# Kernel optimization log

Hardware: AMD Instinct MI355X
Metric: run time of the kernel (lower is better)

## Reference

```python
import jax, jax.numpy as jnp
import numpy as np

N = 30000   # fluid particles
E = 480000  # edges
F = 4       # fluidFeatures (in channels)
P = 8       # RBF basis size per dim (dims=[8], 1D)
LAYERS = [32, 64, 64, 2]


def hat_basis(x, n):
    # 'linear' RBF: hat functions on n evenly spaced centers in [-1, 1]
    centers = jnp.linspace(-1.0, 1.0, n, dtype=x.dtype)
    spacing = 2.0 / (n - 1)
    return jnp.maximum(0.0, 1.0 - jnp.abs(x[:, None] - centers[None, :]) / spacing)  # [E, n]


def rbf_conv(x, fi, fj, d, W, b, mask, n_nodes):
    # x: [N, Cin]; d: [E, 1] clamped; W: [P, Cin, Cout]; b: [Cout]
    phi = hat_basis(d[:, 0], W.shape[0])      # [E, P]
    xj = x[fj]                                 # gather source features [E, Cin]
    msg = jnp.zeros((xj.shape[0], W.shape[2]), dtype=x.dtype)
    for p in range(W.shape[0]):                # small fixed P=8 loop keeps memory O(E*Cout)
        msg = msg + phi[:, p, None] * (xj @ W[p])
    msg = jnp.where(mask[:, None], msg, 0.0)   # centerIgnore: drop self edges fi==fj
    out = jax.ops.segment_sum(msg, fi, num_segments=n_nodes)  # scatter-reduce to targets
    return out + b


def _xavier(key, shape_in, shape_out):
    lim = float(np.sqrt(6.0 / (shape_in + shape_out)))
    return jax.random.uniform(key, (shape_in, shape_out), jnp.float32, -lim, lim)


def setup_inputs() -> dict:
    key = jax.random.key(0)
    ks = jax.random.split(key, 16)
    fluidFeatures = jax.random.normal(ks[0], (N, F), jnp.float32)
    fi = jax.random.randint(ks[1], (E,), 0, N)
    fj = jax.random.randint(ks[2], (E,), 0, N)
    distances = jax.random.normal(ks[3], (E, 1), jnp.float32)
    # conv channels: 4->32, 64->64, 64->64, 64->2
    cio = [(F, 32), (2 * 32, 64), (64, 64), (64, 2)]
    inp = {"fluidFeatures": fluidFeatures, "fi": fi, "fj": fj, "distances": distances}
    for li, (ci, co) in enumerate(cio):
        inp[f"cW{li}"] = jax.random.normal(ks[4 + li], (P, ci, co), jnp.float32) * (1.0 / np.sqrt(P * ci))
        inp[f"cb{li}"] = jnp.zeros((co,), jnp.float32)
        inp[f"fW{li}"] = _xavier(ks[8 + li], ci, co)   # stored [in, out]
        inp[f"fb{li}"] = jnp.zeros((co,), jnp.float32)
    return inp


def reference(fluidFeatures, fi, fj, distances,
              cW0, cb0, fW0, fb0, cW1, cb1, fW1, fb1,
              cW2, cb2, fW2, fb2, cW3, cb3, fW3, fb3):
    n_nodes = fluidFeatures.shape[0]
    mask = fi != fj                     # centerIgnore (mask instead of filter: jit-safe)
    d = jnp.clip(distances, -1.0, 1.0)

    conv0 = rbf_conv(fluidFeatures, fi, fj, d, cW0, cb0, mask, n_nodes)  # [N, 32]
    lin0 = fluidFeatures @ fW0 + fb0                                      # [N, 32]
    ans = jnp.concatenate([lin0, conv0], axis=1)                          # [N, 64]

    # i = 1: features[0]=32 != features[1]=64 -> no residual
    ansc = jax.nn.relu(ans)
    ans = rbf_conv(ansc, fi, fj, d, cW1, cb1, mask, n_nodes) + (ansc @ fW1 + fb1)
    # i = 2: features[1]==features[2]==64 and shapes match -> residual
    ansc = jax.nn.relu(ans)
    ans = rbf_conv(ansc, fi, fj, d, cW2, cb2, mask, n_nodes) + (ansc @ fW2 + fb2) + ans
    # i = 3: 64 -> 2, no residual
    ansc = jax.nn.relu(ans)
    ans = rbf_conv(ansc, fi, fj, d, cW3, cb3, mask, n_nodes) + (ansc @ fW3 + fb3)

    return ans  # dim == 1 (dims=[8]) -> no /128
```

## Files before the change

kernel.cpp:

```cpp
#include <hip/hip_runtime.h>


#define CAP 48

typedef __attribute__((ext_vector_type(8))) short short8;
typedef __attribute__((ext_vector_type(4))) float f32x4;
typedef int v4i __attribute__((ext_vector_type(4)));

__device__ __forceinline__ short bf16s(float f) {
  unsigned u = __float_as_uint(f);
  return (short)((u + 0x7FFF + ((u >> 16) & 1)) >> 16);
}
__device__ __forceinline__ float b2f(unsigned short s) {
  return __uint_as_float(((unsigned)s) << 16);
}
__device__ __forceinline__ unsigned pack2(float a, float b) {
  return (unsigned)(unsigned short)bf16s(a) | ((unsigned)(unsigned short)bf16s(b) << 16);
}
__device__ __forceinline__ float dec_w0(int v) {
  return __uint_as_float(0x3F800000u | (((unsigned)v & 0xFFFu) << 11)) - 1.0f;
}
__device__ __forceinline__ float dec_sf(int v) {
  return (float)(((unsigned)v >> 12) & 1u);
}
__device__ __forceinline__ unsigned long long rfl64(unsigned long long x) {
  unsigned lo = __builtin_amdgcn_readfirstlane((unsigned)x);
  unsigned hi = __builtin_amdgcn_readfirstlane((unsigned)(x >> 32));
  return ((unsigned long long)hi << 32) | (unsigned long long)lo;
}

#define LOAD_RECS32Q(JROW, CPTR, MRAW)                                      \
  v4i q0, q1, q2, q3, q4, q5, q6, q7;                                       \
  int MRAW;                                                                 \
  asm volatile("s_load_dwordx4 %0, %9, 0x0\n\t"                             \
               "s_load_dwordx4 %1, %9, 0x10\n\t"                            \
               "s_load_dwordx4 %2, %9, 0x20\n\t"                            \
               "s_load_dwordx4 %3, %9, 0x30\n\t"                            \
               "s_load_dwordx4 %4, %9, 0x40\n\t"                            \
               "s_load_dwordx4 %5, %9, 0x50\n\t"                            \
               "s_load_dwordx4 %6, %9, 0x60\n\t"                            \
               "s_load_dwordx4 %7, %9, 0x70\n\t"                            \
               "s_load_dword %8, %10, 0x0\n\t"                              \
               "s_waitcnt lgkmcnt(0)"                                       \
               : "=&s"(q0), "=&s"(q1), "=&s"(q2), "=&s"(q3), "=&s"(q4),     \
                 "=&s"(q5), "=&s"(q6), "=&s"(q7), "=&s"(MRAW)               \
               : "s"(JROW), "s"(CPTR)                                       \
               : "memory")

#define LOAD_RECS16TQ(JROW)                                                 \
  v4i qt0, qt1, qt2, qt3;                                                   \
  asm volatile("s_load_dwordx4 %0, %4, 0x80\n\t"                            \
               "s_load_dwordx4 %1, %4, 0x90\n\t"                            \
               "s_load_dwordx4 %2, %4, 0xA0\n\t"                            \
               "s_load_dwordx4 %3, %4, 0xB0\n\t"                            \
               "s_waitcnt lgkmcnt(0)"                                       \
               : "=&s"(qt0), "=&s"(qt1), "=&s"(qt2), "=&s"(qt3)             \
               : "s"(JROW)                                                  \
               : "memory")

#define RECK(K) ((K) < 4 ? q0[(K) & 3] : (K) < 8 ? q1[(K) & 3] :            \
                 (K) < 12 ? q2[(K) & 3] : (K) < 16 ? q3[(K) & 3] :          \
                 (K) < 20 ? q4[(K) & 3] : (K) < 24 ? q5[(K) & 3] :          \
                 (K) < 28 ? q6[(K) & 3] : q7[(K) & 3])
#define RECT(K) ((K) < 4 ? qt0[(K) & 3] : (K) < 8 ? qt1[(K) & 3] :          \
                 (K) < 12 ? qt2[(K) & 3] : qt3[(K) & 3])

__global__ void fill_prep(const float* __restrict__ dist,
                          const int* __restrict__ fi, const int* __restrict__ fj,
                          int* __restrict__ cnt, int* __restrict__ jw, int nE,
                          const float* __restrict__ cW0, const float* __restrict__ fW0,
                          const float* __restrict__ cb0, const float* __restrict__ fb0,
                          const float* __restrict__ cW1, const float* __restrict__ fW1,
                          const float* __restrict__ cb1, const float* __restrict__ fb1,
                          const float* __restrict__ cW2, const float* __restrict__ fW2,
                          const float* __restrict__ cb2, const float* __restrict__ fb2,
                          const float* __restrict__ cW3,
                          short* __restrict__ W0T, short* __restrict__ W1T,
                          short* __restrict__ W2T, short* __restrict__ WT3,
                          float* __restrict__ BIA,
                          const float* __restrict__ X,
                          unsigned short* __restrict__ Xb, int n,
                          int fillBlocks, int prepBlocks) {
  if ((int)blockIdx.x < fillBlocks) {
    int e = blockIdx.x * blockDim.x + threadIdx.x;
    if (e >= nE) return;
    int i = fi[e], j = fj[e];
    if (i == j) return;
    float d = fminf(1.0f, fmaxf(-1.0f, dist[e]));
    float u = (d + 1.0f) * 3.5f;
    int p = min((int)u, 6);
    float w0 = 1.0f - (u - (float)p);
    int wq = min((int)(w0 * 4096.0f + 0.5f), 4095);
    int pos = atomicAdd(&cnt[i], 1);
    if (pos < CAP)
      jw[(size_t)i * CAP + pos] =
          (int)(((unsigned)j << 17) | ((unsigned)p << 14) | 0x1000u | (unsigned)wq);
  } else if ((int)blockIdx.x < fillBlocks + prepBlocks) {
    int idx = ((int)blockIdx.x - fillBlocks) * blockDim.x + threadIdx.x;
    if (idx < 36864) {
      int o = idx / 576, k = idx - o * 576;
      float v = (k < 512) ? cW1[((size_t)(k >> 6) * 64 + (k & 63)) * 64 + o]
                          : fW1[(size_t)(k - 512) * 64 + o];
      W1T[idx] = bf16s(v);
    } else if (idx < 73728) {
      int r = idx - 36864;
      int o = r / 576, k = r - o * 576;
      float v = (k < 512) ? cW2[((size_t)(k >> 6) * 64 + (k & 63)) * 64 + o]
                          : fW2[(size_t)(k - 512) * 64 + o];
      W2T[r] = bf16s(v);
    } else if (idx < 110592) {
      int r = idx - 73728;
      int o = r / 576, k = r - o * 576;
      float v = 0.0f;
      if (k < 512) {
        int s = k >> 6, ci = k & 63;
        if (ci < 4 && o >= 32) v = cW0[((size_t)s * 4 + ci) * 32 + (o - 32)];
      } else {
        int c = k - 512;
        if (c < 4 && o < 32) v = fW0[(size_t)c * 32 + o];
      }
      W0T[r] = bf16s(v);
    } else if (idx < 111616) {
      int r = idx - 110592;
      int t = r >> 6, ch = r & 63;
      WT3[r] = bf16s(cW3[((size_t)(t >> 1) * 64 + ch) * 2 + (t & 1)]);
    } else if (idx < 111808) {
      int r = idx - 111616;
      int layer = r >> 6, ch = r & 63;
      float v;
      if (layer == 0) v = (ch < 32) ? fb0[ch] : cb0[ch - 32];
      else if (layer == 1) v = cb1[ch] + fb1[ch];
      else v = cb2[ch] + fb2[ch];
      BIA[r] = v;
    }
  } else {
    int idx = ((int)blockIdx.x - fillBlocks - prepBlocks) * blockDim.x + threadIdx.x;
    if (idx >= n * 8) return;
    int i = idx >> 3, g = idx & 7;
    uint4 val = make_uint4(0u, 0u, 0u, 0u);
    if (g == 0) {
      float4 x = *(const float4*)(X + (size_t)i * 4);
      val.x = pack2(x.x, x.y);
      val.y = pack2(x.z, x.w);
    }
    *(uint4*)(Xb + (size_t)i * 64 + g * 8) = val;
  }
}

__global__ __launch_bounds__(1024, 8) void conv_agg(
    const unsigned short* __restrict__ prev,
    const int* __restrict__ cnt, const int* __restrict__ jw,
    const short* __restrict__ WTn,
    const float* __restrict__ bias,
    const float* __restrict__ resid,
    float* __restrict__ outF32,
    unsigned short* __restrict__ outAnsc,
    const short* __restrict__ WT3,
    float* __restrict__ T, int flags, int n) {
  __shared__ __align__(16) unsigned short sA[16 * 584];
  __shared__ __align__(16) unsigned short sC[16 * 72];
  const int tid = threadIdx.x;
  const int w = tid >> 6;
  const int lane = tid & 63;
  const unsigned ln2 = (unsigned)lane * 2u;
  const int nodeBase = blockIdx.x * 16;
  const int i = nodeBase + w;
  const bool valid = (i < n);
  const int ic = valid ? i : 0;
  const int* jrow = (const int*)rfl64((unsigned long long)(jw + (size_t)ic * CAP));
  const int* cptr = (const int*)rfl64((unsigned long long)(cnt + ic));
  LOAD_RECS32Q(jrow, cptr, mraw);
  const int m = valid ? min(mraw, CAP) : 0;
  const unsigned short own = prev[(size_t)ic * 64 + lane];
  float aS0 = 0, aS1 = 0, aS2 = 0, aS3 = 0, aS4 = 0, aS5 = 0, aS6 = 0, aS7 = 0;
  unsigned u0, u1, u2, u3, u4, u5, u6, u7;
  unsigned u8, u9, u10, u11, u12, u13, u14, u15;
#define GSETU(G, V) { int v_ = (V);                                         \
    u##G = ((((unsigned)v_) >> 10) & 0xFFFFFF80u) + ln2; }
#define GISSUE16_W8(BASE)                                                   \
  asm volatile("global_load_ushort %0, %0, %[bb]\n\t"                       \
               "global_load_ushort %1, %1, %[bb]\n\t"                       \
               "global_load_ushort %2, %2, %[bb]\n\t"                       \
               "global_load_ushort %3, %3, %[bb]\n\t"                       \
               "global_load_ushort %4, %4, %[bb]\n\t"                       \
               "global_load_ushort %5, %5, %[bb]\n\t"                       \
               "global_load_ushort %6, %6, %[bb]\n\t"                       \
               "global_load_ushort %7, %7, %[bb]\n\t"                       \
               "global_load_ushort %8, %8, %[bb]\n\t"                       \
               "global_load_ushort %9, %9, %[bb]\n\t"                       \
               "global_load_ushort %10, %10, %[bb]\n\t"                     \
               "global_load_ushort %11, %11, %[bb]\n\t"                     \
               "global_load_ushort %12, %12, %[bb]\n\t"                     \
               "global_load_ushort %13, %13, %[bb]\n\t"                     \
               "global_load_ushort %14, %14, %[bb]\n\t"                     \
               "global_load_ushort %15, %15, %[bb]\n\t"                     \
               "s_waitcnt vmcnt(8)"                                         \
               : "+v"(u0), "+v"(u1), "+v"(u2), "+v"(u3),                    \
                 "+v"(u4), "+v"(u5), "+v"(u6), "+v"(u7),                    \
                 "+v"(u8), "+v"(u9), "+v"(u10), "+v"(u11),                  \
                 "+v"(u12), "+v"(u13), "+v"(u14), "+v"(u15)                 \
               : [bb] "s"(BASE)                                             \
               : "memory")
#define WAITV0_HI                                                           \
  asm volatile("s_waitcnt vmcnt(0)"                                         \
               : "+v"(u8), "+v"(u9), "+v"(u10), "+v"(u11),                  \
                 "+v"(u12), "+v"(u13), "+v"(u14), "+v"(u15)                 \
               :: "memory")
#define GCONSU(G, V) { int v_ = (V);                                        \
    float w0_ = dec_w0(v_);                                                 \
    float w1_ = dec_sf(v_) - w0_;                                           \
    float xv_ = __uint_as_float(u##G << 16);                                \
    switch ((((unsigned)v_) >> 14) & 7u) {                                  \
      case 0: aS0 = fmaf(w0_, xv_, aS0); aS1 = fmaf(w1_, xv_, aS1); break;  \
      case 1: aS1 = fmaf(w0_, xv_, aS1); aS2 = fmaf(w1_, xv_, aS2); break;  \
      case 2: aS2 = fmaf(w0_, xv_, aS2); aS3 = fmaf(w1_, xv_, aS3); break;  \
      case 3: aS3 = fmaf(w0_, xv_, aS3); aS4 = fmaf(w1_, xv_, aS4); break;  \
      case 4: aS4 = fmaf(w0_, xv_, aS4); aS5 = fmaf(w1_, xv_, aS5); break;  \
      case 5: aS5 = fmaf(w0_, xv_, aS5); aS6 = fmaf(w1_, xv_, aS6); break;  \
      case 6: aS6 = fmaf(w0_, xv_, aS6); aS7 = fmaf(w1_, xv_, aS7); break;  \
      default: break;                                                       \
    } }
  GSETU(0, RECK(0))   GSETU(1, RECK(1))   GSETU(2, RECK(2))   GSETU(3, RECK(3))
  GSETU(4, RECK(4))   GSETU(5, RECK(5))   GSETU(6, RECK(6))   GSETU(7, RECK(7))
  GSETU(8, RECK(8))   GSETU(9, RECK(9))   GSETU(10, RECK(10)) GSETU(11, RECK(11))
  GSETU(12, RECK(12)) GSETU(13, RECK(13)) GSETU(14, RECK(14)) GSETU(15, RECK(15))
  GISSUE16_W8(prev);
  GCONSU(0, RECK(0)) GCONSU(1, RECK(1)) GCONSU(2, RECK(2)) GCONSU(3, RECK(3))
  GCONSU(4, RECK(4)) GCONSU(5, RECK(5)) GCONSU(6, RECK(6)) GCONSU(7, RECK(7))
  WAITV0_HI;
  GCONSU(8, RECK(8))   GCONSU(9, RECK(9))   GCONSU(10, RECK(10))
  GCONSU(11, RECK(11)) GCONSU(12, RECK(12)) GCONSU(13, RECK(13))
  GCONSU(14, RECK(14)) GCONSU(15, RECK(15))
  if (m > 16) {
    GSETU(0, RECK(16))  GSETU(1, RECK(17))  GSETU(2, RECK(18))  GSETU(3, RECK(19))
    GSETU(4, RECK(20))  GSETU(5, RECK(21))  GSETU(6, RECK(22))  GSETU(7, RECK(23))
    GSETU(8, RECK(24))  GSETU(9, RECK(25))  GSETU(10, RECK(26)) GSETU(11, RECK(27))
    GSETU(12, RECK(28)) GSETU(13, RECK(29)) GSETU(14, RECK(30)) GSETU(15, RECK(31))
    GISSUE16_W8(prev);
    GCONSU(0, RECK(16)) GCONSU(1, RECK(17)) GCONSU(2, RECK(18)) GCONSU(3, RECK(19))
    GCONSU(4, RECK(20)) GCONSU(5, RECK(21)) GCONSU(6, RECK(22)) GCONSU(7, RECK(23))
    WAITV0_HI;
    GCONSU(8, RECK(24))  GCONSU(9, RECK(25))  GCONSU(10, RECK(26))
    GCONSU(11, RECK(27)) GCONSU(12, RECK(28)) GCONSU(13, RECK(29))
    GCONSU(14, RECK(30)) GCONSU(15, RECK(31))
    if (m > 32) {
      LOAD_RECS16TQ(jrow);
      GSETU(0, RECT(0))   GSETU(1, RECT(1))   GSETU(2, RECT(2))   GSETU(3, RECT(3))
      GSETU(4, RECT(4))   GSETU(5, RECT(5))   GSETU(6, RECT(6))   GSETU(7, RECT(7))
      GSETU(8, RECT(8))   GSETU(9, RECT(9))   GSETU(10, RECT(10)) GSETU(11, RECT(11))
      GSETU(12, RECT(12)) GSETU(13, RECT(13)) GSETU(14, RECT(14)) GSETU(15, RECT(15))
      GISSUE16_W8(prev);
      GCONSU(0, RECT(0)) GCONSU(1, RECT(1)) GCONSU(2, RECT(2)) GCONSU(3, RECT(3))
      GCONSU(4, RECT(4)) GCONSU(5, RECT(5)) GCONSU(6, RECT(6)) GCONSU(7, RECT(7))
      WAITV0_HI;
      GCONSU(8, RECT(8))   GCONSU(9, RECT(9))   GCONSU(10, RECT(10))
      GCONSU(11, RECT(11)) GCONSU(12, RECT(12)) GCONSU(13, RECT(13))
      GCONSU(14, RECT(14)) GCONSU(15, RECT(15))
    }
  }
#undef GSETU
#undef GISSUE16_W8
#undef WAITV0_HI
#undef GCONSU
  {
    unsigned short* sAr = sA + w * 584;
    sAr[0 * 64 + lane] = (unsigned short)bf16s(aS0);
    sAr[1 * 64 + lane] = (unsigned short)bf16s(aS1);
    sAr[2 * 64 + lane] = (unsigned short)bf16s(aS2);
    sAr[3 * 64 + lane] = (unsigned short)bf16s(aS3);
    sAr[4 * 64 + lane] = (unsigned short)bf16s(aS4);
    sAr[5 * 64 + lane] = (unsigned short)bf16s(aS5);
    sAr[6 * 64 + lane] = (unsigned short)bf16s(aS6);
    sAr[7 * 64 + lane] = (unsigned short)bf16s(aS7);
    sAr[512 + lane] = own;
  }
  __syncthreads();

  if (w < 4) {
    const int mrow = lane & 15, quad = lane >> 4, t = w;
    const unsigned rowoff = (unsigned)((t * 16 + mrow) * 1152 + quad * 16);
    const unsigned short* brow = sA + mrow * 584 + quad * 8;
    f32x4 acc4 = {0, 0, 0, 0};
    short8 f0, f1, f2, f3, f4, f5;
#define WLOAD6(CO)                                                          \
  asm volatile("global_load_dwordx4 %0, %[vo], %[bb] offset:0\n\t"          \
               "global_load_dwordx4 %1, %[vo], %[bb] offset:64\n\t"         \
               "global_load_dwordx4 %2, %[vo], %[bb] offset:128\n\t"        \
               "global_load_dwordx4 %3, %[vo], %[bb] offset:192\n\t"        \
               "global_load_dwordx4 %4, %[vo], %[bb] offset:256\n\t"        \
               "global_load_dwordx4 %5, %[vo], %[bb] offset:320\n\t"        \
               "s_waitcnt vmcnt(0)"                                         \
               : "=&v"(f0), "=&v"(f1), "=&v"(f2), "=&v"(f3),                \
                 "=&v"(f4), "=&v"(f5)                                       \
               : [vo] "v"(rowoff + (CO)), [bb] "s"(WTn)                     \
               : "memory")
#define MM6(KK0)                                                            \
  acc4 = __builtin_amdgcn_mfma_f32_16x16x32_bf16(                           \
      f0, *(const short8*)(brow + ((KK0) + 0) * 32), acc4, 0, 0, 0);        \
  acc4 = __builtin_amdgcn_mfma_f32_16x16x32_bf16(                           \
      f1, *(const short8*)(brow + ((KK0) + 1) * 32), acc4, 0, 0, 0);        \
  acc4 = __builtin_amdgcn_mfma_f32_16x16x32_bf16(                           \
      f2, *(const short8*)(brow + ((KK0) + 2) * 32), acc4, 0, 0, 0);        \
  acc4 = __builtin_amdgcn_mfma_f32_16x16x32_bf16(                           \
      f3, *(const short8*)(brow + ((KK0) + 3) * 32), acc4, 0, 0, 0);        \
  acc4 = __builtin_amdgcn_mfma_f32_16x16x32_bf16(                           \
      f4, *(const short8*)(brow + ((KK0) + 4) * 32), acc4, 0, 0, 0);        \
  acc4 = __builtin_amdgcn_mfma_f32_16x16x32_bf16(                           \
      f5, *(const short8*)(brow + ((KK0) + 5) * 32), acc4, 0, 0, 0);
    WLOAD6(0);    MM6(0);
    WLOAD6(384);  MM6(6);
    WLOAD6(768);  MM6(12);
#undef WLOAD6
#undef MM6
    const int node2 = nodeBase + mrow;
    const int ch0 = t * 16 + quad * 4;
    if (node2 < n) {
      float4 bb4 = *(const float4*)(bias + ch0);
      float4 rv = make_float4(0.f, 0.f, 0.f, 0.f);
      if (flags & 1) rv = *(const float4*)(resid + (size_t)node2 * 64 + ch0);
      float o0 = acc4[0] + bb4.x + rv.x;
      float o1 = acc4[1] + bb4.y + rv.y;
      float o2 = acc4[2] + bb4.z + rv.z;
      float o3 = acc4[3] + bb4.w + rv.w;
      if (flags & 2) {
        *(float2*)(outF32 + (size_t)node2 * 64 + ch0) = make_float2(o0, o1);
        *(float2*)(outF32 + (size_t)node2 * 64 + ch0 + 2) = make_float2(o2, o3);
      }
      unsigned lo = pack2(fmaxf(o0, 0.f), fmaxf(o1, 0.f));
      unsigned hi = pack2(fmaxf(o2, 0.f), fmaxf(o3, 0.f));
      *(uint2*)(outAnsc + (size_t)node2 * 64 + ch0) = make_uint2(lo, hi);
      if (flags & 4) {
        *(unsigned*)(sC + mrow * 72 + ch0) = lo;
        *(unsigned*)(sC + mrow * 72 + ch0 + 2) = hi;
      }
    } else if (flags & 4) {
      *(unsigned*)(sC + mrow * 72 + ch0) = 0u;
      *(unsigned*)(sC + mrow * 72 + ch0 + 2) = 0u;
    }
  }
  if (flags & 4) {
    __syncthreads();
    if (w == 0) {
      const int mrow = lane & 15, quad = lane >> 4;
      short8 b0 = *(const short8*)(sC + mrow * 72 + quad * 8);
      short8 b1 = *(const short8*)(sC + mrow * 72 + quad * 8 + 32);
      short8 a0v = *(const short8*)(WT3 + mrow * 64 + quad * 8);
      short8 a1v = *(const short8*)(WT3 + mrow * 64 + quad * 8 + 32);
      f32x4 acc4 = {0, 0, 0, 0};
      acc4 = __builtin_amdgcn_mfma_f32_16x16x32_bf16(a0v, b0, acc4, 0, 0, 0);
      acc4 = __builtin_amdgcn_mfma_f32_16x16x32_bf16(a1v, b1, acc4, 0, 0, 0);
      const int node2 = nodeBase + mrow;
      if (node2 < n) {
        float* tr = T + (size_t)node2 * 18 + quad * 4;
        *(float2*)(tr) = make_float2(acc4[0], acc4[1]);
        *(float2*)(tr + 2) = make_float2(acc4[2], acc4[3]);
      }
    }
  }
}

__global__ __launch_bounds__(256, 4) void layer3_kernel(
    const unsigned short* __restrict__ Xb,
    const float* __restrict__ T,
    const int* __restrict__ cnt, const int* __restrict__ jw,
    const float* __restrict__ cb3, const float* __restrict__ fb3,
    const float* __restrict__ fW3,
    float* __restrict__ out, int n) {
  const int lane = threadIdx.x & 63;
  const int i = (blockIdx.x * blockDim.x + threadIdx.x) >> 6;
  if (i >= n) return;
  const int m = min(cnt[i], CAP);
  float c0 = 0.0f, c1 = 0.0f;
  if (lane < m) {
    int v = jw[(size_t)i * CAP + lane];
    unsigned j = (unsigned)v >> 17;
    unsigned p = ((unsigned)v >> 14) & 7u;
    unsigned off9 = j * 9u + p;
    float w0 = dec_w0(v);
    float w1 = 1.0f - w0;
    const float* tb = T + (size_t)off9 * 2;
    float2 ta = *(const float2*)(tb);
    float2 tc = *(const float2*)(tb + 2);
    c0 = w0 * ta.x + w1 * tc.x;
    c1 = w0 * ta.y + w1 * tc.y;
  }
  float xi = b2f(Xb[(size_t)i * 64 + lane]);
  float2 fw = *(const float2*)(fW3 + lane * 2);
  c0 = fmaf(xi, fw.x, c0);
  c1 = fmaf(xi, fw.y, c1);
  #pragma unroll
  for (int off = 32; off > 0; off >>= 1) {
    c0 += __shfl_xor(c0, off, 64);
    c1 += __shfl_xor(c1, off, 64);
  }
  if (lane == 0) {
    out[(size_t)i * 2 + 0] = c0 + cb3[0] + fb3[0];
    out[(size_t)i * 2 + 1] = c1 + cb3[1] + fb3[1];
  }
}

extern "C" void kernel_launch(void* const* d_in, const int* in_sizes, int n_in,
                              void* d_out, int out_size, void* d_ws, size_t ws_size,
                              hipStream_t stream) {
  const float* X    = (const float*)d_in[0];
  const int*   fi   = (const int*)d_in[1];
  const int*   fj   = (const int*)d_in[2];
  const float* dist = (const float*)d_in[3];
  const float* cW0 = (const float*)d_in[4];  const float* cb0 = (const float*)d_in[5];
  const float* fW0 = (const float*)d_in[6];  const float* fb0 = (const float*)d_in[7];
  const float* cW1 = (const float*)d_in[8];  const float* cb1 = (const float*)d_in[9];
  const float* fW1 = (const float*)d_in[10]; const float* fb1 = (const float*)d_in[11];
  const float* cW2 = (const float*)d_in[12]; const float* cb2 = (const float*)d_in[13];
  const float* fW2 = (const float*)d_in[14]; const float* fb2 = (const float*)d_in[15];
  const float* cW3 = (const float*)d_in[16]; const float* cb3 = (const float*)d_in[17];
  const float* fW3 = (const float*)d_in[18]; const float* fb3 = (const float*)d_in[19];
  float* out = (float*)d_out;

  const int n  = in_sizes[0] / 4;
  const int nE = in_sizes[1];

  unsigned short* ansc0 = (unsigned short*)d_ws;
  float*          ans1  = (float*)(ansc0 + (size_t)n * 64);
  unsigned short* ansc1 = (unsigned short*)(ans1 + (size_t)n * 64);
  unsigned short* ansc2 = ansc1 + (size_t)n * 64;
  float*          T     = (float*)(ansc2 + (size_t)n * 64);
  unsigned short* Xb16  = (unsigned short*)(T + (size_t)n * 18);
  short* W1T = (short*)(Xb16 + (size_t)n * 64);
  short* W2T = W1T + 36864;
  short* W0T = W2T + 36864;
  short* WT3 = W0T + 36864;
  float* BIA = (float*)(WT3 + 1024);
  int*   jw  = (int*)(BIA + 192);
  int*   cnt = jw + (size_t)n * CAP;

  hipMemsetAsync(jw, 0, ((size_t)n * CAP + n) * sizeof(int), stream);
  const int fillBlocks = (nE + 255) / 256;
  const int prepBlocks = (111808 + 255) / 256;
  const int xbBlocks   = (n * 8 + 255) / 256;
  fill_prep<<<fillBlocks + prepBlocks + xbBlocks, 256, 0, stream>>>(
      dist, fi, fj, cnt, jw, nE,
      cW0, fW0, cb0, fb0, cW1, fW1, cb1, fb1, cW2, fW2, cb2, fb2, cW3,
      W0T, W1T, W2T, WT3, BIA, X, Xb16, n, fillBlocks, prepBlocks);

  const int nodeBlocks = (n + 15) / 16;
  conv_agg<<<nodeBlocks, 1024, 0, stream>>>(Xb16, cnt, jw, W0T, BIA,
                                            ans1, ans1, ansc0, WT3, T, 0, n);
  conv_agg<<<nodeBlocks, 1024, 0, stream>>>(ansc0, cnt, jw, W1T, BIA + 64,
                                            ans1, ans1, ansc1, WT3, T, 2, n);
  conv_agg<<<nodeBlocks, 1024, 0, stream>>>(ansc1, cnt, jw, W2T, BIA + 128,
                                            ans1, ans1, ansc2, WT3, T, 5, n);
  layer3_kernel<<<(n * 64 + 255) / 256, 256, 0, stream>>>(ansc2, T, cnt, jw,
                                                          cb3, fb3, fW3, out, n);
}
```

Before: 249.4 us.

## Bucket edges by RBF bin and accumulate sorted runs in conv_agg

Edge records are first bucketed per node by basis index p into a 128-slot staging array, then a new compact kernel writes them into the per-node CAP list sorted by p. conv_agg then walks edges in p order with two running accumulators and flushes them to shared memory on each bin change, replacing the 8-way switch over eight accumulator registers. Edges past the count are masked, and the weight quantisation grows to 14 bits. This adds a kernel launch and extra staging memory traffic, and the flush branches may diverge across edges.

Result: no change. 245.5 us (-1.6%).

```diff
diff --git a/kernel.cpp b/kernel.cpp
--- a/kernel.cpp
+++ b/kernel.cpp
@@ -17,11 +17,8 @@
 __device__ __forceinline__ unsigned pack2(float a, float b) {
   return (unsigned)(unsigned short)bf16s(a) | ((unsigned)(unsigned short)bf16s(b) << 16);
 }
-__device__ __forceinline__ float dec_w0(int v) {
-  return __uint_as_float(0x3F800000u | (((unsigned)v & 0xFFFu) << 11)) - 1.0f;
-}
-__device__ __forceinline__ float dec_sf(int v) {
-  return (float)(((unsigned)v >> 12) & 1u);
+__device__ __forceinline__ float dec14(int v) {
+  return __uint_as_float(0x3F800000u | (((unsigned)v & 0x3FFFu) << 9)) - 1.0f;
 }
 __device__ __forceinline__ unsigned long long rfl64(unsigned long long x) {
   unsigned lo = __builtin_amdgcn_readfirstlane((unsigned)x);
@@ -67,7 +64,7 @@
 
 __global__ void fill_prep(const float* __restrict__ dist,
                           const int* __restrict__ fi, const int* __restrict__ fj,
-                          int* __restrict__ cnt, int* __restrict__ jw, int nE,
+                          int* __restrict__ cnt8, int* __restrict__ jwB, int nE,
                           const float* __restrict__ cW0, const float* __restrict__ fW0,
                           const float* __restrict__ cb0, const float* __restrict__ fb0,
                           const float* __restrict__ cW1, const float* __restrict__ fW1,
@@ -90,11 +87,11 @@
     float u = (d + 1.0f) * 3.5f;
     int p = min((int)u, 6);
     float w0 = 1.0f - (u - (float)p);
-    int wq = min((int)(w0 * 4096.0f + 0.5f), 4095);
-    int pos = atomicAdd(&cnt[i], 1);
-    if (pos < CAP)
-      jw[(size_t)i * CAP + pos] =
-          (int)(((unsigned)j << 17) | ((unsigned)p << 14) | 0x1000u | (unsigned)wq);
+    int wq = min((int)(w0 * 16384.0f + 0.5f), 16383);
+    int pos = atomicAdd(&cnt8[i * 8 + p], 1);
+    if (pos < 16)
+      jwB[(size_t)i * 128 + p * 16 + pos] =
+          (int)(((unsigned)j << 17) | ((unsigned)p << 14) | (unsigned)wq);
   } else if ((int)blockIdx.x < fillBlocks + prepBlocks) {
     int idx = ((int)blockIdx.x - fillBlocks) * blockDim.x + threadIdx.x;
     if (idx < 36864) {
@@ -147,6 +144,34 @@
   }
 }
 
+__global__ __launch_bounds__(256, 8) void compact_kernel(
+    const int* __restrict__ jwB, const int* __restrict__ cnt8,
+    int* __restrict__ jw, int* __restrict__ cnt, int n) {
+  const int w = threadIdx.x >> 6, lane = threadIdx.x & 63;
+  const int i = blockIdx.x * 4 + w;
+  if (i >= n) return;
+  const int4* c8 = (const int4*)(cnt8 + (size_t)i * 8);
+  int4 ca = c8[0], cb = c8[1];
+  int c0 = min(ca.x, 16), c1 = min(ca.y, 16), c2 = min(ca.z, 16), c3 = min(ca.w, 16);
+  int c4 = min(cb.x, 16), c5 = min(cb.y, 16), c6 = min(cb.z, 16), c7 = min(cb.w, 16);
+  int tot = c0 + c1 + c2 + c3 + c4 + c5 + c6 + c7;
+  if (lane == 0) cnt[i] = min(tot, CAP);
+  #pragma unroll
+  for (int h = 0; h < 2; ++h) {
+    int s = lane + h * 64;
+    int p = s >> 4, k = s & 15;
+    int cp = p == 0 ? c0 : p == 1 ? c1 : p == 2 ? c2 : p == 3 ? c3
+           : p == 4 ? c4 : p == 5 ? c5 : p == 6 ? c6 : c7;
+    int ps = (p > 0 ? c0 : 0) + (p > 1 ? c1 : 0) + (p > 2 ? c2 : 0) +
+             (p > 3 ? c3 : 0) + (p > 4 ? c4 : 0) + (p > 5 ? c5 : 0) +
+             (p > 6 ? c6 : 0);
+    if (k < cp) {
+      int pos = ps + k;
+      if (pos < CAP) jw[(size_t)i * CAP + pos] = jwB[(size_t)i * 128 + s];
+    }
+  }
+}
+
 __global__ __launch_bounds__(1024, 8) void conv_agg(
     const unsigned short* __restrict__ prev,
     const int* __restrict__ cnt, const int* __restrict__ jw,
@@ -170,13 +195,18 @@
   const int* jrow = (const int*)rfl64((unsigned long long)(jw + (size_t)ic * CAP));
   const int* cptr = (const int*)rfl64((unsigned long long)(cnt + ic));
   LOAD_RECS32Q(jrow, cptr, mraw);
-  const int m = valid ? min(mraw, CAP) : 0;
+  const int mloc = valid ? min(mraw, CAP) : 0;
   const unsigned short own = prev[(size_t)ic * 64 + lane];
-  float aS0 = 0, aS1 = 0, aS2 = 0, aS3 = 0, aS4 = 0, aS5 = 0, aS6 = 0, aS7 = 0;
+  unsigned short* sAr = sA + w * 584;
+  #pragma unroll
+  for (int r = 0; r < 8; ++r) sAr[r * 64 + lane] = 0;
+  sAr[512 + lane] = own;
   unsigned u0, u1, u2, u3, u4, u5, u6, u7;
   unsigned u8, u9, u10, u11, u12, u13, u14, u15;
-#define GSETU(G, V) { int v_ = (V);                                         \
-    u##G = ((((unsigned)v_) >> 10) & 0xFFFFFF80u) + ln2; }
+#define GSETU(G, KCMP, RV)                                                  \
+  { unsigned o_ = ((KCMP) < mloc)                                           \
+        ? ((((unsigned)(RV)) >> 10) & 0xFFFFFF80u) : 0u;                    \
+    u##G = o_ + ln2; }
 #define GISSUE16_W8(BASE)                                                   \
   asm volatile("global_load_ushort %0, %0, %[bb]\n\t"                       \
                "global_load_ushort %1, %1, %[bb]\n\t"                       \
@@ -206,74 +236,80 @@
                : "+v"(u8), "+v"(u9), "+v"(u10), "+v"(u11),                  \
                  "+v"(u12), "+v"(u13), "+v"(u14), "+v"(u15)                 \
                :: "memory")
-#define GCONSU(G, V) { int v_ = (V);                                        \
-    float w0_ = dec_w0(v_);                                                 \
-    float w1_ = dec_sf(v_) - w0_;                                           \
+#define CONSK(KCMP, G, RV)                                                  \
+  if ((KCMP) == mloc) goto cons_done;                                       \
+  { int v_ = (RV);                                                          \
+    int pk_ = (v_ >> 14) & 7;                                               \
+    if (pk_ != pcur) {                                                      \
+      sAr[pcur * 64 + lane] = (unsigned short)bf16s(curA);                  \
+      if (pk_ == pcur + 1) { curA = curB; }                                 \
+      else { sAr[(pcur + 1) * 64 + lane] = (unsigned short)bf16s(curB);     \
+             curA = 0.0f; }                                                 \
+      curB = 0.0f; pcur = pk_;                                              \
+    }                                                                       \
+    float f_ = __uint_as_float(0x3F800000u | (((unsigned)v_ & 0x3FFFu) << 9)); \
     float xv_ = __uint_as_float(u##G << 16);                                \
-    switch ((((unsigned)v_) >> 14) & 7u) {                                  \
-      case 0: aS0 = fmaf(w0_, xv_, aS0); aS1 = fmaf(w1_, xv_, aS1); break;  \
-      case 1: aS1 = fmaf(w0_, xv_, aS1); aS2 = fmaf(w1_, xv_, aS2); break;  \
-      case 2: aS2 = fmaf(w0_, xv_, aS2); aS3 = fmaf(w1_, xv_, aS3); break;  \
-      case 3: aS3 = fmaf(w0_, xv_, aS3); aS4 = fmaf(w1_, xv_, aS4); break;  \
-      case 4: aS4 = fmaf(w0_, xv_, aS4); aS5 = fmaf(w1_, xv_, aS5); break;  \
-      case 5: aS5 = fmaf(w0_, xv_, aS5); aS6 = fmaf(w1_, xv_, aS6); break;  \
-      case 6: aS6 = fmaf(w0_, xv_, aS6); aS7 = fmaf(w1_, xv_, aS7); break;  \
-      default: break;                                                       \
-    } }
-  GSETU(0, RECK(0))   GSETU(1, RECK(1))   GSETU(2, RECK(2))   GSETU(3, RECK(3))
-  GSETU(4, RECK(4))   GSETU(5, RECK(5))   GSETU(6, RECK(6))   GSETU(7, RECK(7))
-  GSETU(8, RECK(8))   GSETU(9, RECK(9))   GSETU(10, RECK(10)) GSETU(11, RECK(11))
-  GSETU(12, RECK(12)) GSETU(13, RECK(13)) GSETU(14, RECK(14)) GSETU(15, RECK(15))
-  GISSUE16_W8(prev);
-  GCONSU(0, RECK(0)) GCONSU(1, RECK(1)) GCONSU(2, RECK(2)) GCONSU(3, RECK(3))
-  GCONSU(4, RECK(4)) GCONSU(5, RECK(5)) GCONSU(6, RECK(6)) GCONSU(7, RECK(7))
-  WAITV0_HI;
-  GCONSU(8, RECK(8))   GCONSU(9, RECK(9))   GCONSU(10, RECK(10))
-  GCONSU(11, RECK(11)) GCONSU(12, RECK(12)) GCONSU(13, RECK(13))
-  GCONSU(14, RECK(14)) GCONSU(15, RECK(15))
-  if (m > 16) {
-    GSETU(0, RECK(16))  GSETU(1, RECK(17))  GSETU(2, RECK(18))  GSETU(3, RECK(19))
-    GSETU(4, RECK(20))  GSETU(5, RECK(21))  GSETU(6, RECK(22))  GSETU(7, RECK(23))
-    GSETU(8, RECK(24))  GSETU(9, RECK(25))  GSETU(10, RECK(26)) GSETU(11, RECK(27))
-    GSETU(12, RECK(28)) GSETU(13, RECK(29)) GSETU(14, RECK(30)) GSETU(15, RECK(31))
+    curA = fmaf(f_ - 1.0f, xv_, curA);                                      \
+    curB = fmaf(2.0f - f_, xv_, curB);                                      \
+  }
+  if (mloc > 0) {
+    int pcur = (RECK(0) >> 14) & 7;
+    float curA = 0.0f, curB = 0.0f;
+    GSETU(0, 0, RECK(0))    GSETU(1, 1, RECK(1))    GSETU(2, 2, RECK(2))
+    GSETU(3, 3, RECK(3))    GSETU(4, 4, RECK(4))    GSETU(5, 5, RECK(5))
+    GSETU(6, 6, RECK(6))    GSETU(7, 7, RECK(7))    GSETU(8, 8, RECK(8))
+    GSETU(9, 9, RECK(9))    GSETU(10, 10, RECK(10)) GSETU(11, 11, RECK(11))
+    GSETU(12, 12, RECK(12)) GSETU(13, 13, RECK(13)) GSETU(14, 14, RECK(14))
+    GSETU(15, 15, RECK(15))
     GISSUE16_W8(prev);
-    GCONSU(0, RECK(16)) GCONSU(1, RECK(17)) GCONSU(2, RECK(18)) GCONSU(3, RECK(19))
-    GCONSU(4, RECK(20)) GCONSU(5, RECK(21)) GCONSU(6, RECK(22)) GCONSU(7, RECK(23))
+    CONSK(0, 0, RECK(0))   CONSK(1, 1, RECK(1))   CONSK(2, 2, RECK(2))
+    CONSK(3, 3, RECK(3))   CONSK(4, 4, RECK(4))   CONSK(5, 5, RECK(5))
+    CONSK(6, 6, RECK(6))   CONSK(7, 7, RECK(7))
     WAITV0_HI;
-    GCONSU(8, RECK(24))  GCONSU(9, RECK(25))  GCONSU(10, RECK(26))
-    GCONSU(11, RECK(27)) GCONSU(12, RECK(28)) GCONSU(13, RECK(29))
-    GCONSU(14, RECK(30)) GCONSU(15, RECK(31))
-    if (m > 32) {
-      LOAD_RECS16TQ(jrow);
-      GSETU(0, RECT(0))   GSETU(1, RECT(1))   GSETU(2, RECT(2))   GSETU(3, RECT(3))
-      GSETU(4, RECT(4))   GSETU(5, RECT(5))   GSETU(6, RECT(6))   GSETU(7, RECT(7))
-      GSETU(8, RECT(8))   GSETU(9, RECT(9))   GSETU(10, RECT(10)) GSETU(11, RECT(11))
-      GSETU(12, RECT(12)) GSETU(13, RECT(13)) GSETU(14, RECT(14)) GSETU(15, RECT(15))
+    CONSK(8, 8, RECK(8))   CONSK(9, 9, RECK(9))   CONSK(10, 10, RECK(10))
+    CONSK(11, 11, RECK(11)) CONSK(12, 12, RECK(12)) CONSK(13, 13, RECK(13))
+    CONSK(14, 14, RECK(14)) CONSK(15, 15, RECK(15))
+    if (mloc > 16) {
+      GSETU(0, 16, RECK(16))  GSETU(1, 17, RECK(17))  GSETU(2, 18, RECK(18))
+      GSETU(3, 19, RECK(19))  GSETU(4, 20, RECK(20))  GSETU(5, 21, RECK(21))
+      GSETU(6, 22, RECK(22))  GSETU(7, 23, RECK(23))  GSETU(8, 24, RECK(24))
+      GSETU(9, 25, RECK(25))  GSETU(10, 26, RECK(26)) GSETU(11, 27, RECK(27))
+      GSETU(12, 28, RECK(28)) GSETU(13, 29, RECK(29)) GSETU(14, 30, RECK(30))
+      GSETU(15, 31, RECK(31))
       GISSUE16_W8(prev);
-      GCONSU(0, RECT(0)) GCONSU(1, RECT(1)) GCONSU(2, RECT(2)) GCONSU(3, RECT(3))
-      GCONSU(4, RECT(4)) GCONSU(5, RECT(5)) GCONSU(6, RECT(6)) GCONSU(7, RECT(7))
+      CONSK(16, 0, RECK(16))  CONSK(17, 1, RECK(17))  CONSK(18, 2, RECK(18))
+      CONSK(19, 3, RECK(19))  CONSK(20, 4, RECK(20))  CONSK(21, 5, RECK(21))
+      CONSK(22, 6, RECK(22))  CONSK(23, 7, RECK(23))
       WAITV0_HI;
-      GCONSU(8, RECT(8))   GCONSU(9, RECT(9))   GCONSU(10, RECT(10))
-      GCONSU(11, RECT(11)) GCONSU(12, RECT(12)) GCONSU(13, RECT(13))
-      GCONSU(14, RECT(14)) GCONSU(15, RECT(15))
-    }
+      CONSK(24, 8, RECK(24))  CONSK(25, 9, RECK(25))  CONSK(26, 10, RECK(26))
+      CONSK(27, 11, RECK(27)) CONSK(28, 12, RECK(28)) CONSK(29, 13, RECK(29))
+      CONSK(30, 14, RECK(30)) CONSK(31, 15, RECK(31))
+      if (mloc > 32) {
+        LOAD_RECS16TQ(jrow);
+        GSETU(0, 32, RECT(0))   GSETU(1, 33, RECT(1))   GSETU(2, 34, RECT(2))
+        GSETU(3, 35, RECT(3))   GSETU(4, 36, RECT(4))   GSETU(5, 37, RECT(5))
+        GSETU(6, 38, RECT(6))   GSETU(7, 39, RECT(7))   GSETU(8, 40, RECT(8))
+        GSETU(9, 41, RECT(9))   GSETU(10, 42, RECT(10)) GSETU(11, 43, RECT(11))
+        GSETU(12, 44, RECT(12)) GSETU(13, 45, RECT(13)) GSETU(14, 46, RECT(14))
+        GSETU(15, 47, RECT(15))
+        GISSUE16_W8(prev);
+        CONSK(32, 0, RECT(0))   CONSK(33, 1, RECT(1))   CONSK(34, 2, RECT(2))
+        CONSK(35, 3, RECT(3))   CONSK(36, 4, RECT(4))   CONSK(37, 5, RECT(5))
+        CONSK(38, 6, RECT(6))   CONSK(39, 7, RECT(7))
+        WAITV0_HI;
+        CONSK(40, 8, RECT(8))   CONSK(41, 9, RECT(9))   CONSK(42, 10, RECT(10))
+        CONSK(43, 11, RECT(11)) CONSK(44, 12, RECT(12)) CONSK(45, 13, RECT(13))
+        CONSK(46, 14, RECT(14)) CONSK(47, 15, RECT(15))
+      }
+    }
+cons_done: ;
+    sAr[pcur * 64 + lane] = (unsigned short)bf16s(curA);
+    sAr[(pcur + 1) * 64 + lane] = (unsigned short)bf16s(curB);
   }
 #undef GSETU
 #undef GISSUE16_W8
 #undef WAITV0_HI
-#undef GCONSU
-  {
-    unsigned short* sAr = sA + w * 584;
-    sAr[0 * 64 + lane] = (unsigned short)bf16s(aS0);
-    sAr[1 * 64 + lane] = (unsigned short)bf16s(aS1);
-    sAr[2 * 64 + lane] = (unsigned short)bf16s(aS2);
-    sAr[3 * 64 + lane] = (unsigned short)bf16s(aS3);
-    sAr[4 * 64 + lane] = (unsigned short)bf16s(aS4);
-    sAr[5 * 64 + lane] = (unsigned short)bf16s(aS5);
-    sAr[6 * 64 + lane] = (unsigned short)bf16s(aS6);
-    sAr[7 * 64 + lane] = (unsigned short)bf16s(aS7);
-    sAr[512 + lane] = own;
-  }
+#undef CONSK
   __syncthreads();
 
   if (w < 4) {
@@ -376,7 +412,7 @@
     unsigned j = (unsigned)v >> 17;
     unsigned p = ((unsigned)v >> 14) & 7u;
     unsigned off9 = j * 9u + p;
-    float w0 = dec_w0(v);
+    float w0 = dec14(v);
     float w1 = 1.0f - w0;
     const float* tb = T + (size_t)off9 * 2;
     float2 ta = *(const float2*)(tb);
@@ -430,17 +466,21 @@
   short* W0T = W2T + 36864;
   short* WT3 = W0T + 36864;
   float* BIA = (float*)(WT3 + 1024);
-  int*   jw  = (int*)(BIA + 192);
-  int*   cnt = jw + (size_t)n * CAP;
-
-  hipMemsetAsync(jw, 0, ((size_t)n * CAP + n) * sizeof(int), stream);
+  int*   jw   = (int*)(BIA + 192);
+  int*   cnt  = jw + (size_t)n * CAP;
+  int*   jwB  = cnt + n;
+  int*   cnt8 = jwB + (size_t)n * 128;
+
+  hipMemsetAsync(cnt8, 0, (size_t)n * 8 * sizeof(int), stream);
   const int fillBlocks = (nE + 255) / 256;
   const int prepBlocks = (111808 + 255) / 256;
   const int xbBlocks   = (n * 8 + 255) / 256;
   fill_prep<<<fillBlocks + prepBlocks + xbBlocks, 256, 0, stream>>>(
-      dist, fi, fj, cnt, jw, nE,
+      dist, fi, fj, cnt8, jwB, nE,
       cW0, fW0, cb0, fb0, cW1, fW1, cb1, fb1, cW2, fW2, cb2, fb2, cW3,
       W0T, W1T, W2T, WT3, BIA, X, Xb16, n, fillBlocks, prepBlocks);
+
+  compact_kernel<<<(n + 3) / 4, 256, 0, stream>>>(jwB, cnt8, jw, cnt, n);
 
   const int nodeBlocks = (n + 15) / 16;
   conv_agg<<<nodeBlocks, 1024, 0, stream>>>(Xb16, cnt, jw, W0T, BIA,
```
